# Performance work log

Measured on AMD Instinct MI355X. Metric: run time of the kernel, lower is better.

Reference implementation:

```python
import jax, jax.numpy as jnp
import numpy as np
import math

D_MODEL = 1024
NUM_HEADS = 16
HEAD_DIM = D_MODEL // NUM_HEADS
CLAMP = 1e9


def setup_inputs() -> dict:
    key = jax.random.key(0)
    k1, k2, k3, k4, k5 = jax.random.split(key, 5)
    B, S = 2, 2048
    x = jax.random.normal(k1, (B, S, D_MODEL), dtype=jnp.float32)
    # torch Linear params, stored as [in, out] (y = x @ W + b)
    s1 = 1.0 / math.sqrt(D_MODEL)
    W_qkv = jax.random.uniform(k2, (D_MODEL, 3 * D_MODEL), jnp.float32, -s1, s1)
    b_qkv = jax.random.uniform(k3, (3 * D_MODEL,), jnp.float32, -s1, s1)
    W_out = jax.random.uniform(k4, (D_MODEL, D_MODEL), jnp.float32, -s1, s1)
    b_out = jax.random.uniform(k5, (D_MODEL,), jnp.float32, -s1, s1)
    return {"x": x, "W_qkv": W_qkv, "b_qkv": b_qkv, "W_out": W_out, "b_out": b_out}


def reference(x, W_qkv, b_qkv, W_out, b_out):
    B, S, D = x.shape
    qkv = x @ W_qkv + b_qkv                       # [B, S, 3*D]
    qkv = qkv.reshape(B, S, NUM_HEADS, 3 * HEAD_DIM).transpose(0, 2, 1, 3)  # [B, H, S, 3*hd]
    q, k, v = jnp.split(qkv, 3, axis=-1)          # each [B, H, S, hd]
    scale = 1.0 / math.sqrt(HEAD_DIM)
    scores = jnp.einsum('bhqd,bhkd->bhqk', q, k) * scale  # [B, H, S, S]
    causal = jnp.tril(jnp.ones((S, S), dtype=bool))
    scores = jnp.where(causal, scores, -jnp.inf)
    scores = jnp.clip(scores, -CLAMP, CLAMP)      # -inf -> -1e9, matching torch clamp
    attn = jax.nn.softmax(scores, axis=-1)
    values = jnp.einsum('bhqk,bhkd->bhqd', attn, v)        # [B, H, S, hd]
    values = values.transpose(0, 2, 1, 3).reshape(B, S, D)  # [B, S, D]
    out = values @ W_out + b_out
    # dropout is identity in eval mode
    return out
```

## Files before the change

kernel.cpp:

```cpp
#include <hip/hip_runtime.h>
#include <hip/hip_bf16.h>

#define D_MODEL 1024
#define NUM_HEADS 16
#define HEAD_DIM 64
#define SEQ 2048
#define BATCH 2
#define ROWS (BATCH * SEQ)

typedef unsigned short u16;
typedef __bf16 bf16x8 __attribute__((ext_vector_type(8)));
typedef float f32x4 __attribute__((ext_vector_type(4)));

__device__ inline u16 f2bfu(float f) {
  unsigned u = __float_as_uint(f);
  unsigned r = (u + 0x7fffu + ((u >> 16) & 1u)) >> 16;
  return (u16)r;
}

__device__ inline unsigned cvt_pk_bf16(float a, float b) {
#if __has_builtin(__builtin_amdgcn_cvt_pk_bf16_f32)
  auto r = __builtin_amdgcn_cvt_pk_bf16_f32(a, b);
  unsigned u;
  __builtin_memcpy(&u, &r, 4);
  return u;
#else
  return (unsigned)f2bfu(a) | ((unsigned)f2bfu(b) << 16);
#endif
}

__device__ inline f32x4 mfma16(bf16x8 a, bf16x8 b, f32x4 c) {
  return __builtin_amdgcn_mfma_f32_16x16x32_bf16(a, b, c, 0, 0, 0);
}

__device__ inline bf16x8 load_frag(const u16* p) {
  union { uint4 v; bf16x8 f; } u;
  u.v = *(const uint4*)p;
  return u.f;
}

__device__ inline void gload_lds16(const u16* g, u16* l) {
  __builtin_amdgcn_global_load_lds((const __attribute__((address_space(1))) void*)g,
                                   (__attribute__((address_space(3))) void*)l, 16, 0, 0);
}


__global__ __launch_bounds__(256) void cvt_x_kernel(const float* __restrict__ x,
                                                    u16* __restrict__ y) {
  int i = blockIdx.x * 256 + threadIdx.x;
  float4 v = ((const float4*)x)[i];
  uint2 o;
  o.x = cvt_pk_bf16(v.x, v.y);
  o.y = cvt_pk_bf16(v.z, v.w);
  ((uint2*)y)[i] = o;
}

__global__ __launch_bounds__(256) void transpose_cvt(const float* __restrict__ W,
                                                     u16* __restrict__ Wt,
                                                     int K, int N) {
  __shared__ float t[32][33];
  int k0 = blockIdx.x * 32, n0 = blockIdx.y * 32;
  int c = threadIdx.x & 31, r8 = threadIdx.x >> 5;
#pragma unroll
  for (int i = 0; i < 4; i++) {
    int r = r8 + i * 8;
    t[r][c] = W[(size_t)(k0 + r) * N + n0 + c];
  }
  __syncthreads();
#pragma unroll
  for (int i = 0; i < 4; i++) {
    int r = r8 + i * 8;
    Wt[(size_t)(n0 + r) * K + k0 + c] = f2bfu(t[c][r]);
  }
}


__global__ __launch_bounds__(256, 3) void gemm_qkv(const u16* __restrict__ A,
                                                   const u16* __restrict__ Bt,
                                                   const float* __restrict__ bias,
                                                   u16* __restrict__ Qb, u16* __restrict__ Kb,
                                                   u16* __restrict__ Vt) {
  __shared__ u16 lA0[128 * 32], lB0[128 * 32];
  __shared__ u16 lA1[128 * 32], lB1[128 * 32];
  const int tid = threadIdx.x;
  const int wave = tid >> 6, lane = tid & 63, ln = lane & 15, quad = lane >> 4;
  const int n0 = blockIdx.x * 128, m0 = blockIdx.y * 128;
  const int wm = (wave & 1) * 64, wn = (wave >> 1) * 64;
  f32x4 acc[4][4] = {};

  auto issue = [&](u16* dA, u16* dB, int k0) {
#pragma unroll
    for (int i = 0; i < 2; ++i) {
      int rb = wave * 2 + i;
      gload_lds16(A + (size_t)(m0 + rb * 16 + ln) * 1024 + k0 + quad * 8, dA + rb * 512);
      gload_lds16(Bt + (size_t)(n0 + rb * 16 + ln) * 1024 + k0 + quad * 8, dB + rb * 512);
    }
  };
  auto compute = [&](const u16* sA, const u16* sB) {
    bf16x8 a[4], b[4];
#pragma unroll
    for (int i = 0; i < 4; ++i) {
      a[i] = load_frag(sA + (wm / 16 + i) * 512 + quad * 128 + ln * 8);
      b[i] = load_frag(sB + (wn / 16 + i) * 512 + quad * 128 + ln * 8);
    }
#pragma unroll
    for (int mt = 0; mt < 4; ++mt)
#pragma unroll
      for (int nt = 0; nt < 4; ++nt) acc[mt][nt] = mfma16(a[mt], b[nt], acc[mt][nt]);
  };

  issue(lA0, lB0, 0);
  for (int p = 0; p < 15; ++p) {
    asm volatile("s_barrier" ::: "memory");
    issue(lA1, lB1, (2 * p + 1) * 32);
    asm volatile("s_waitcnt vmcnt(4)" ::: "memory");
    asm volatile("s_barrier" ::: "memory");
    compute(lA0, lB0);
    asm volatile("s_barrier" ::: "memory");
    issue(lA0, lB0, (2 * p + 2) * 32);
    asm volatile("s_waitcnt vmcnt(4)" ::: "memory");
    asm volatile("s_barrier" ::: "memory");
    compute(lA1, lB1);
  }
  asm volatile("s_barrier" ::: "memory");
  issue(lA1, lB1, 31 * 32);
  asm volatile("s_waitcnt vmcnt(4)" ::: "memory");
  asm volatile("s_barrier" ::: "memory");
  compute(lA0, lB0);
  asm volatile("s_waitcnt vmcnt(0)" ::: "memory");
  asm volatile("s_barrier" ::: "memory");
  compute(lA1, lB1);

#pragma unroll
  for (int mt = 0; mt < 4; ++mt) {
    int row = m0 + wm + mt * 16 + quad * 4;
    int bb = row >> 11, s0 = row & 2047;
#pragma unroll
    for (int nt = 0; nt < 4; ++nt) {
      int col = n0 + wn + nt * 16 + ln;
      float bv = bias[col];
      int h = col / 192, rem = col - h * 192, t3 = rem >> 6, d = rem & 63;
      int bh = bb * NUM_HEADS + h;
      if (t3 == 2) {
        uint2 pk;
        pk.x = cvt_pk_bf16(acc[mt][nt][0] + bv, acc[mt][nt][1] + bv);
        pk.y = cvt_pk_bf16(acc[mt][nt][2] + bv, acc[mt][nt][3] + bv);
        *(uint2*)(Vt + ((size_t)bh * 64 + d) * SEQ + s0) = pk;
      } else {
        u16* dst = (t3 == 0) ? Qb : Kb;
#pragma unroll
        for (int r = 0; r < 4; ++r)
          dst[((size_t)bh * SEQ + s0 + r) * 64 + d] = f2bfu(acc[mt][nt][r] + bv);
      }
    }
  }
}


__global__ __launch_bounds__(512) void attn_kernel(const u16* __restrict__ Qb,
                                                   const u16* __restrict__ Kb,
                                                   const u16* __restrict__ Vt,
                                                   u16* __restrict__ Ob) {
  __shared__ u16 lK[64 * 64];
  __shared__ u16 lV[64 * 64];
  __shared__ u16 lP[8][2048];
  const int tid = threadIdx.x;
  const int wave = tid >> 6, lane = tid & 63;
  const int ln = lane & 15, quad = lane >> 4;
  const int j = blockIdx.x;
  const int lo = j, hi = 31 - j;
  const int myt = (wave < 4) ? lo : hi;
  const int q0w = myt * 64 + (wave & 3) * 16;
  const int ktend = myt;
  const int bh = blockIdx.y;
  const u16* Qg = Qb + (size_t)bh * SEQ * 64;
  const u16* Kg = Kb + (size_t)bh * SEQ * 64;
  const u16* Vg = Vt + (size_t)bh * 64 * SEQ;
  u16* lPw = lP[wave];

  const u16* sp[2];
  u16* dp[2];
  const int sstride = (wave < 4) ? 64 * 64 : 64;
#pragma unroll
  for (int i = 0; i < 2; ++i) {
    int c = wave * 2 + i;
    if (c < 8) {
      int rb = c >> 1, kgh = c & 1;
      sp[i] = Kg + (size_t)(rb * 16 + ln) * 64 + (kgh * 4 + quad) * 8;
      dp[i] = lK + rb * 1024 + kgh * 512;
    } else {
      int cc = c - 8, rb = cc >> 1, kgh = cc & 1;
      sp[i] = Vg + (size_t)(rb * 16 + ln) * SEQ + (kgh * 4 + quad) * 8;
      dp[i] = lV + rb * 1024 + kgh * 512;
    }
  }

  bf16x8 qf[2];
#pragma unroll
  for (int ks = 0; ks < 2; ++ks)
    qf[ks] = load_frag(Qg + (size_t)(q0w + ln) * 64 + ks * 32 + quad * 8);

  f32x4 o[4] = {};
  float m_r = -1e30f;
  float l_r = 0.f;
  const float SC = 0.18033688011112042f;
  const int qq = q0w + ln;

  for (int kt = 0; kt <= hi; ++kt) {
    __syncthreads();
#pragma unroll
    for (int i = 0; i < 2; ++i) gload_lds16(sp[i], dp[i]);
#pragma unroll
    for (int i = 0; i < 2; ++i) sp[i] += sstride;
    __syncthreads();

    if (kt <= ktend) {
      f32x4 sc[4] = {};
#pragma unroll
      for (int mt = 0; mt < 4; ++mt) {
#pragma unroll
        for (int ks = 0; ks < 2; ++ks) {
          bf16x8 kf = load_frag(lK + mt * 1024 + (ks * 4 + quad) * 128 + ln * 8);
          sc[mt] = mfma16(kf, qf[ks], sc[mt]);
        }
      }
      if (kt == ktend) {
#pragma unroll
        for (int mt = 0; mt < 4; ++mt) {
          int key0 = kt * 64 + mt * 16 + quad * 4;
#pragma unroll
          for (int r = 0; r < 4; ++r)
            if (key0 + r > qq) sc[mt][r] = -1e30f;
        }
      }
      float mloc = sc[0][0];
#pragma unroll
      for (int mt = 0; mt < 4; ++mt)
#pragma unroll
        for (int r = 0; r < 4; ++r) mloc = fmaxf(mloc, sc[mt][r]);
      mloc = fmaxf(mloc, __shfl_xor(mloc, 16));
      mloc = fmaxf(mloc, __shfl_xor(mloc, 32));
      float mnew = fmaxf(m_r, mloc);
      float alpha = __builtin_amdgcn_exp2f((m_r - mnew) * SC);
      float nmsc = -mnew * SC;
      float sum = 0.f;
#pragma unroll
      for (int mt = 0; mt < 4; ++mt)
#pragma unroll
        for (int r = 0; r < 4; ++r) {
          float p = __builtin_amdgcn_exp2f(__builtin_fmaf(sc[mt][r], SC, nmsc));
          sc[mt][r] = p;
          sum += p;
        }
      sum += __shfl_xor(sum, 16);
      sum += __shfl_xor(sum, 32);
      l_r = l_r * alpha + sum;
      m_r = mnew;
#pragma unroll
      for (int dt = 0; dt < 4; ++dt) o[dt] *= alpha;

#pragma unroll
      for (int mt = 0; mt < 4; ++mt) {
        uint2 pk;
        pk.x = cvt_pk_bf16(sc[mt][0], sc[mt][1]);
        pk.y = cvt_pk_bf16(sc[mt][2], sc[mt][3]);
        int addr = ln * 64 + (((mt * 2 + (quad >> 1)) ^ (ln & 7)) * 8) + (quad & 1) * 4;
        *(uint2*)(lPw + addr) = pk;
      }
      bf16x8 pf[2];
#pragma unroll
      for (int ks = 0; ks < 2; ++ks)
        pf[ks] = load_frag(lPw + ln * 64 + (((ks * 4 + quad) ^ (ln & 7)) * 8));
#pragma unroll
      for (int dt = 0; dt < 4; ++dt) {
#pragma unroll
        for (int ks = 0; ks < 2; ++ks) {
          bf16x8 av = load_frag(lV + dt * 1024 + (ks * 4 + quad) * 128 + ln * 8);
          o[dt] = mfma16(av, pf[ks], o[dt]);
        }
      }
    }
  }

  float inv = 1.f / l_r;
#pragma unroll
  for (int dt = 0; dt < 4; ++dt) {
    uint2 pk;
    pk.x = cvt_pk_bf16(o[dt][0] * inv, o[dt][1] * inv);
    pk.y = cvt_pk_bf16(o[dt][2] * inv, o[dt][3] * inv);
    *(uint2*)(lPw + ln * 72 + dt * 16 + quad * 4) = pk;
  }
  const int b = bh >> 4, h = bh & 15;
#pragma unroll
  for (int i = 0; i < 2; ++i) {
    int c = lane + i * 64;
    int qq2 = c >> 3, dg = c & 7;
    uint4 val = *(const uint4*)(lPw + qq2 * 72 + dg * 8);
    *(uint4*)(Ob + ((size_t)b * SEQ + q0w + qq2) * 1024 + h * 64 + dg * 8) = val;
  }
}


__global__ __launch_bounds__(256) void gemm_out(const u16* __restrict__ A,
                                                const u16* __restrict__ Bt,
                                                const float* __restrict__ bias,
                                                float* __restrict__ out) {
  __shared__ u16 lA[64 * 64];
  __shared__ u16 lB[64 * 64];
  const int tid = threadIdx.x;
  const int wave = tid >> 6, lane = tid & 63, ln = lane & 15, quad = lane >> 4;
  const int n0 = blockIdx.x * 64, m0 = blockIdx.y * 64;
  const int wm = (wave & 1) * 32, wn = (wave >> 1) * 32;
  f32x4 acc[2][2] = {};

  for (int kt = 0; kt < 16; ++kt) {
    const int k0 = kt * 64;
    __syncthreads();
#pragma unroll
    for (int i = 0; i < 4; ++i) {
      int c = wave * 4 + i;
      if (c < 8) {
        int rb = c >> 1, kgh = c & 1;
        gload_lds16(A + (size_t)(m0 + rb * 16 + ln) * 1024 + k0 + (kgh * 4 + quad) * 8,
                    lA + rb * 1024 + kgh * 512);
      } else {
        int cc = c - 8, rb = cc >> 1, kgh = cc & 1;
        gload_lds16(Bt + (size_t)(n0 + rb * 16 + ln) * 1024 + k0 + (kgh * 4 + quad) * 8,
                    lB + rb * 1024 + kgh * 512);
      }
    }
    __syncthreads();
#pragma unroll
    for (int ks = 0; ks < 2; ++ks) {
      bf16x8 a[2], b[2];
#pragma unroll
      for (int i = 0; i < 2; ++i) {
        a[i] = load_frag(lA + (wm / 16 + i) * 1024 + (ks * 4 + quad) * 128 + ln * 8);
        b[i] = load_frag(lB + (wn / 16 + i) * 1024 + (ks * 4 + quad) * 128 + ln * 8);
      }
#pragma unroll
      for (int mt = 0; mt < 2; ++mt)
#pragma unroll
        for (int nt = 0; nt < 2; ++nt) acc[mt][nt] = mfma16(a[mt], b[nt], acc[mt][nt]);
    }
  }
#pragma unroll
  for (int mt = 0; mt < 2; ++mt) {
    int row = m0 + wm + mt * 16 + quad * 4;
#pragma unroll
    for (int nt = 0; nt < 2; ++nt) {
      int col = n0 + wn + nt * 16 + ln;
      float bv = bias[col];
#pragma unroll
      for (int r = 0; r < 4; ++r)
        out[(size_t)(row + r) * 1024 + col] = acc[mt][nt][r] + bv;
    }
  }
}


extern "C" void kernel_launch(void* const* d_in, const int* in_sizes, int n_in,
                              void* d_out, int out_size, void* d_ws, size_t ws_size,
                              hipStream_t stream) {
  const float* x = (const float*)d_in[0];
  const float* W_qkv = (const float*)d_in[1];
  const float* b_qkv = (const float*)d_in[2];
  const float* W_out = (const float*)d_in[3];
  const float* b_out = (const float*)d_in[4];
  float* out = (float*)d_out;

  char* ws = (char*)d_ws;
  const size_t SZ_XB = (size_t)ROWS * D_MODEL * 2;
  const size_t SZ_WQKVT = (size_t)3 * D_MODEL * D_MODEL * 2;
  const size_t SZ_WOUTT = (size_t)D_MODEL * D_MODEL * 2;
  const size_t SZ_HEADS = (size_t)BATCH * NUM_HEADS * SEQ * HEAD_DIM * 2;
  u16* xb = (u16*)(ws);
  u16* WqkvT = (u16*)(ws + SZ_XB);
  u16* WoutT = (u16*)(ws + SZ_XB + SZ_WQKVT);
  u16* Qb = (u16*)(ws + SZ_XB + SZ_WQKVT + SZ_WOUTT);
  u16* Kb = (u16*)(ws + SZ_XB + SZ_WQKVT + SZ_WOUTT + SZ_HEADS);
  u16* Vt = (u16*)(ws + SZ_XB + SZ_WQKVT + SZ_WOUTT + 2 * SZ_HEADS);
  u16* Ob = (u16*)(ws + SZ_XB + SZ_WQKVT + SZ_WOUTT + 3 * SZ_HEADS);

  cvt_x_kernel<<<dim3(ROWS * D_MODEL / 4 / 256), dim3(256), 0, stream>>>(x, xb);
  transpose_cvt<<<dim3(D_MODEL / 32, 3 * D_MODEL / 32), dim3(256), 0, stream>>>(W_qkv, WqkvT,
                                                                                D_MODEL, 3 * D_MODEL);
  transpose_cvt<<<dim3(D_MODEL / 32, D_MODEL / 32), dim3(256), 0, stream>>>(W_out, WoutT,
                                                                            D_MODEL, D_MODEL);
  gemm_qkv<<<dim3(3 * D_MODEL / 128, ROWS / 128), dim3(256), 0, stream>>>(xb, WqkvT, b_qkv,
                                                                          Qb, Kb, Vt);
  attn_kernel<<<dim3(SEQ / 128, BATCH * NUM_HEADS), dim3(512), 0, stream>>>(Qb, Kb, Vt, Ob);
  gemm_out<<<dim3(D_MODEL / 64, ROWS / 64), dim3(256), 0, stream>>>(Ob, WoutT, b_out, out);
}
```

Before: 228.7 us.

## Double-buffer K/V loads in attention and pipeline output GEMM with larger tiles

```diff
diff --git a/kernel.cpp b/kernel.cpp
--- a/kernel.cpp
+++ b/kernel.cpp
@@ -161,9 +161,9 @@
                                                    const u16* __restrict__ Kb,
                                                    const u16* __restrict__ Vt,
                                                    u16* __restrict__ Ob) {
-  __shared__ u16 lK[64 * 64];
-  __shared__ u16 lV[64 * 64];
-  __shared__ u16 lP[8][2048];
+  __shared__ u16 lK0[64 * 64], lV0[64 * 64];
+  __shared__ u16 lK1[64 * 64], lV1[64 * 64];
+  __shared__ u16 lP[8][1152];
   const int tid = threadIdx.x;
   const int wave = tid >> 6, lane = tid & 63;
   const int ln = lane & 15, quad = lane >> 4;
@@ -178,8 +178,13 @@
   const u16* Vg = Vt + (size_t)bh * 64 * SEQ;
   u16* lPw = lP[wave];
 
+  bf16x8 qf[2];
+#pragma unroll
+  for (int ks = 0; ks < 2; ++ks)
+    qf[ks] = load_frag(Qg + (size_t)(q0w + ln) * 64 + ks * 32 + quad * 8);
+
   const u16* sp[2];
-  u16* dp[2];
+  u16 *dpa[2], *dpb[2];
   const int sstride = (wave < 4) ? 64 * 64 : 64;
 #pragma unroll
   for (int i = 0; i < 2; ++i) {
@@ -187,18 +192,15 @@
     if (c < 8) {
       int rb = c >> 1, kgh = c & 1;
       sp[i] = Kg + (size_t)(rb * 16 + ln) * 64 + (kgh * 4 + quad) * 8;
-      dp[i] = lK + rb * 1024 + kgh * 512;
+      dpa[i] = lK0 + rb * 1024 + kgh * 512;
+      dpb[i] = lK1 + rb * 1024 + kgh * 512;
     } else {
       int cc = c - 8, rb = cc >> 1, kgh = cc & 1;
       sp[i] = Vg + (size_t)(rb * 16 + ln) * SEQ + (kgh * 4 + quad) * 8;
-      dp[i] = lV + rb * 1024 + kgh * 512;
-    }
-  }
-
-  bf16x8 qf[2];
-#pragma unroll
-  for (int ks = 0; ks < 2; ++ks)
-    qf[ks] = load_frag(Qg + (size_t)(q0w + ln) * 64 + ks * 32 + quad * 8);
+      dpa[i] = lV0 + rb * 1024 + kgh * 512;
+      dpb[i] = lV1 + rb * 1024 + kgh * 512;
+    }
+  }
 
   f32x4 o[4] = {};
   float m_r = -1e30f;
@@ -206,21 +208,31 @@
   const float SC = 0.18033688011112042f;
   const int qq = q0w + ln;
 
+  gload_lds16(sp[0], dpa[0]);
+  gload_lds16(sp[1], dpa[1]);
+  sp[0] += sstride; sp[1] += sstride;
+
   for (int kt = 0; kt <= hi; ++kt) {
-    __syncthreads();
-#pragma unroll
-    for (int i = 0; i < 2; ++i) gload_lds16(sp[i], dp[i]);
-#pragma unroll
-    for (int i = 0; i < 2; ++i) sp[i] += sstride;
-    __syncthreads();
+    asm volatile("s_barrier" ::: "memory");
+    if (kt < hi) {
+      if (kt & 1) { gload_lds16(sp[0], dpa[0]); gload_lds16(sp[1], dpa[1]); }
+      else        { gload_lds16(sp[0], dpb[0]); gload_lds16(sp[1], dpb[1]); }
+      sp[0] += sstride; sp[1] += sstride;
+      asm volatile("s_waitcnt vmcnt(2)" ::: "memory");
+    } else {
+      asm volatile("s_waitcnt vmcnt(0)" ::: "memory");
+    }
+    asm volatile("s_barrier" ::: "memory");
 
     if (kt <= ktend) {
+      const u16* cK = (kt & 1) ? lK1 : lK0;
+      const u16* cV = (kt & 1) ? lV1 : lV0;
       f32x4 sc[4] = {};
 #pragma unroll
       for (int mt = 0; mt < 4; ++mt) {
 #pragma unroll
         for (int ks = 0; ks < 2; ++ks) {
-          bf16x8 kf = load_frag(lK + mt * 1024 + (ks * 4 + quad) * 128 + ln * 8);
+          bf16x8 kf = load_frag(cK + mt * 1024 + (ks * 4 + quad) * 128 + ln * 8);
           sc[mt] = mfma16(kf, qf[ks], sc[mt]);
         }
       }
@@ -275,7 +287,7 @@
       for (int dt = 0; dt < 4; ++dt) {
 #pragma unroll
         for (int ks = 0; ks < 2; ++ks) {
-          bf16x8 av = load_frag(lV + dt * 1024 + (ks * 4 + quad) * 128 + ln * 8);
+          bf16x8 av = load_frag(cV + dt * 1024 + (ks * 4 + quad) * 128 + ln * 8);
           o[dt] = mfma16(av, pf[ks], o[dt]);
         }
       }
@@ -301,55 +313,71 @@
 }
 
 
-__global__ __launch_bounds__(256) void gemm_out(const u16* __restrict__ A,
-                                                const u16* __restrict__ Bt,
-                                                const float* __restrict__ bias,
-                                                float* __restrict__ out) {
-  __shared__ u16 lA[64 * 64];
-  __shared__ u16 lB[64 * 64];
+__global__ __launch_bounds__(256, 3) void gemm_out(const u16* __restrict__ A,
+                                                   const u16* __restrict__ Bt,
+                                                   const float* __restrict__ bias,
+                                                   float* __restrict__ out) {
+  __shared__ u16 lA0[128 * 32], lB0[64 * 32];
+  __shared__ u16 lA1[128 * 32], lB1[64 * 32];
   const int tid = threadIdx.x;
   const int wave = tid >> 6, lane = tid & 63, ln = lane & 15, quad = lane >> 4;
-  const int n0 = blockIdx.x * 64, m0 = blockIdx.y * 64;
-  const int wm = (wave & 1) * 32, wn = (wave >> 1) * 32;
-  f32x4 acc[2][2] = {};
-
-  for (int kt = 0; kt < 16; ++kt) {
-    const int k0 = kt * 64;
-    __syncthreads();
-#pragma unroll
-    for (int i = 0; i < 4; ++i) {
-      int c = wave * 4 + i;
+  const int n0 = blockIdx.x * 64, m0 = blockIdx.y * 128;
+  f32x4 acc[2][4] = {};
+
+  auto issue = [&](u16* dA, u16* dB, int k0) {
+#pragma unroll
+    for (int i = 0; i < 3; ++i) {
+      int c = wave * 3 + i;
       if (c < 8) {
-        int rb = c >> 1, kgh = c & 1;
-        gload_lds16(A + (size_t)(m0 + rb * 16 + ln) * 1024 + k0 + (kgh * 4 + quad) * 8,
-                    lA + rb * 1024 + kgh * 512);
+        gload_lds16(A + (size_t)(m0 + c * 16 + ln) * 1024 + k0 + quad * 8, dA + c * 512);
       } else {
-        int cc = c - 8, rb = cc >> 1, kgh = cc & 1;
-        gload_lds16(Bt + (size_t)(n0 + rb * 16 + ln) * 1024 + k0 + (kgh * 4 + quad) * 8,
-                    lB + rb * 1024 + kgh * 512);
-      }
-    }
-    __syncthreads();
-#pragma unroll
-    for (int ks = 0; ks < 2; ++ks) {
-      bf16x8 a[2], b[2];
-#pragma unroll
-      for (int i = 0; i < 2; ++i) {
-        a[i] = load_frag(lA + (wm / 16 + i) * 1024 + (ks * 4 + quad) * 128 + ln * 8);
-        b[i] = load_frag(lB + (wn / 16 + i) * 1024 + (ks * 4 + quad) * 128 + ln * 8);
-      }
-#pragma unroll
-      for (int mt = 0; mt < 2; ++mt)
-#pragma unroll
-        for (int nt = 0; nt < 2; ++nt) acc[mt][nt] = mfma16(a[mt], b[nt], acc[mt][nt]);
-    }
-  }
+        int cc = c - 8;
+        gload_lds16(Bt + (size_t)(n0 + cc * 16 + ln) * 1024 + k0 + quad * 8, dB + cc * 512);
+      }
+    }
+  };
+  auto compute = [&](const u16* sA, const u16* sB) {
+    bf16x8 a[2], b[4];
+#pragma unroll
+    for (int i = 0; i < 2; ++i)
+      a[i] = load_frag(sA + (wave * 2 + i) * 512 + quad * 128 + ln * 8);
+#pragma unroll
+    for (int i = 0; i < 4; ++i)
+      b[i] = load_frag(sB + i * 512 + quad * 128 + ln * 8);
+#pragma unroll
+    for (int mt = 0; mt < 2; ++mt)
+#pragma unroll
+      for (int nt = 0; nt < 4; ++nt) acc[mt][nt] = mfma16(a[mt], b[nt], acc[mt][nt]);
+  };
+
+  issue(lA0, lB0, 0);
+  for (int p = 0; p < 15; ++p) {
+    asm volatile("s_barrier" ::: "memory");
+    issue(lA1, lB1, (2 * p + 1) * 32);
+    asm volatile("s_waitcnt vmcnt(3)" ::: "memory");
+    asm volatile("s_barrier" ::: "memory");
+    compute(lA0, lB0);
+    asm volatile("s_barrier" ::: "memory");
+    issue(lA0, lB0, (2 * p + 2) * 32);
+    asm volatile("s_waitcnt vmcnt(3)" ::: "memory");
+    asm volatile("s_barrier" ::: "memory");
+    compute(lA1, lB1);
+  }
+  asm volatile("s_barrier" ::: "memory");
+  issue(lA1, lB1, 31 * 32);
+  asm volatile("s_waitcnt vmcnt(3)" ::: "memory");
+  asm volatile("s_barrier" ::: "memory");
+  compute(lA0, lB0);
+  asm volatile("s_waitcnt vmcnt(0)" ::: "memory");
+  asm volatile("s_barrier" ::: "memory");
+  compute(lA1, lB1);
+
 #pragma unroll
   for (int mt = 0; mt < 2; ++mt) {
-    int row = m0 + wm + mt * 16 + quad * 4;
-#pragma unroll
-    for (int nt = 0; nt < 2; ++nt) {
-      int col = n0 + wn + nt * 16 + ln;
+    int row = m0 + wave * 32 + mt * 16 + quad * 4;
+#pragma unroll
+    for (int nt = 0; nt < 4; ++nt) {
+      int col = n0 + nt * 16 + ln;
       float bv = bias[col];
 #pragma unroll
       for (int r = 0; r < 4; ++r)
@@ -390,5 +418,5 @@
   gemm_qkv<<<dim3(3 * D_MODEL / 128, ROWS / 128), dim3(256), 0, stream>>>(xb, WqkvT, b_qkv,
                                                                           Qb, Kb, Vt);
   attn_kernel<<<dim3(SEQ / 128, BATCH * NUM_HEADS), dim3(512), 0, stream>>>(Qb, Kb, Vt, Ob);
-  gemm_out<<<dim3(D_MODEL / 64, ROWS / 64), dim3(256), 0, stream>>>(Ob, WoutT, b_out, out);
-}
+  gemm_out<<<dim3(D_MODEL / 64, ROWS / 128), dim3(256), 0, stream>>>(Ob, WoutT, b_out, out);
+}
```

Measured after the change: 221.6 us. -3.1%, faster.
